# Performance work log

Measured on AMD Instinct MI355X. Metric: run time of the kernel, lower is better.

Reference implementation:

```python
import math
import jax
import jax.numpy as jnp
import numpy as np

B, S, S_IMG, D, H, MAX_SEQ = 8, 1024, 1, 1024, 16, 1024
HD = D // H


def setup_inputs() -> dict:
    key = jax.random.key(0)
    ks = jax.random.split(key, 8)
    w = 0.02  # GPT-2 init scale keeps softmax well-conditioned
    return {
        "hidden_states": jax.random.normal(ks[0], (B, S, D), jnp.float32),
        "attention_mask": jnp.ones((B, 1, 1, S + S_IMG), jnp.float32),
        "image_hidden_states": jax.random.normal(ks[1], (B, S_IMG, D), jnp.float32),
        "Wc_attn": jax.random.normal(ks[2], (D, 3 * D), jnp.float32) * w,  # Conv1D: x @ W + b
        "bc_attn": jnp.zeros((3 * D,), jnp.float32),
        "Wc_proj": jax.random.normal(ks[3], (D, D), jnp.float32) * w,
        "bc_proj": jnp.zeros((D,), jnp.float32),
        "Wuk": jax.random.normal(ks[4], (D, D), jnp.float32) * w,  # nn.Linear weight: x @ W.T
        "Wuv": jax.random.normal(ks[5], (D, D), jnp.float32) * w,
    }


def _split_heads(x):
    b, s, _ = x.shape
    return x.reshape(b, s, H, HD).transpose(0, 2, 1, 3)  # [B,H,S,hd]


def reference(hidden_states, attention_mask, image_hidden_states,
              Wc_attn, bc_attn, Wc_proj, bc_proj, Wuk, Wuv):
    # c_attn (Conv1D): x @ W + b, then split into q,k,v
    qkv = hidden_states @ Wc_attn + bc_attn
    q, k, v = jnp.split(qkv, 3, axis=-1)
    q, k, v = _split_heads(q), _split_heads(k), _split_heads(v)

    # image KV via bias-free Linear layers, appended to text KV (layer_past=None)
    k_img = _split_heads(image_hidden_states @ Wuk.T)
    v_img = _split_heads(image_hidden_states @ Wuv.T)
    k = jnp.concatenate([k, k_img], axis=2)
    v = jnp.concatenate([v, v_img], axis=2)

    Q, K = q.shape[2], k.shape[2]
    scores = jnp.einsum("bhqd,bhkd->bhqk", q, k) / math.sqrt(HD)

    # causal mask: tril(ones(max_seq_len, max_seq_len+1)) sliced to [Q,K]
    causal = jnp.tril(jnp.ones((MAX_SEQ, MAX_SEQ + 1), bool))[None, None, :Q, :K]
    scores = jnp.where(causal, scores, jnp.float32(-1e9))
    scores = jnp.where(attention_mask == 0, jnp.float32(-1e4), scores)

    p_attn = jax.nn.softmax(scores, axis=-1)  # dropout p=0 -> identity
    x = jnp.einsum("bhqk,bhkd->bhqd", p_attn, v)
    x = x.transpose(0, 2, 1, 3).reshape(hidden_states.shape[0], Q, D)
    return x @ Wc_proj + bc_proj
```

## Files before the change

### kernel.cpp

```cpp
#include <hip/hip_runtime.h>


#define DEVINL __device__ __forceinline__

typedef __attribute__((ext_vector_type(8))) short bf16x8;
typedef __attribute__((ext_vector_type(4))) float f32x4;
typedef __attribute__((ext_vector_type(16))) float f32x16;
typedef __attribute__((ext_vector_type(4))) unsigned int u32x4;

DEVINL unsigned short f2bf(float f) {
  unsigned u = __float_as_uint(f);
  u += 0x7fffu + ((u >> 16) & 1u);
  return (unsigned short)(u >> 16);
}

DEVINL void gload_lds16(const void* g, void* l) {
  __builtin_amdgcn_global_load_lds(
      (const __attribute__((address_space(1))) void*)g,
      (__attribute__((address_space(3))) void*)l, 16, 0, 0);
}

#define BARRIER() asm volatile("s_barrier" ::: "memory")

__global__ void cast_f32_bf16(const float* __restrict__ in,
                              unsigned short* __restrict__ out, int n4) {
  int i = blockIdx.x * blockDim.x + threadIdx.x;
  if (i >= n4) return;
  float4 f = ((const float4*)in)[i];
  uint2 o;
  o.x = (unsigned)f2bf(f.x) | ((unsigned)f2bf(f.y) << 16);
  o.y = (unsigned)f2bf(f.z) | ((unsigned)f2bf(f.w) << 16);
  ((uint2*)out)[i] = o;
}

__global__ void transpose_cast(const float* __restrict__ in,
                               unsigned short* __restrict__ out,
                               int rows, int cols) {
  __shared__ unsigned short tile[32][33];
  int bx = blockIdx.x * 32, by = blockIdx.y * 32;
  int tx = threadIdx.x, ty = threadIdx.y;
#pragma unroll
  for (int i = 0; i < 32; i += 8)
    tile[ty + i][tx] = f2bf(in[(size_t)(by + ty + i) * cols + bx + tx]);
  __syncthreads();
#pragma unroll
  for (int i = 0; i < 32; i += 8)
    out[(size_t)(bx + ty + i) * rows + by + tx] = tile[tx][ty + i];
}


DEVINL void stage_tile(const unsigned short* __restrict__ A,
                       const unsigned short* __restrict__ Bt, int m0, int n0,
                       int kt, int buf, int t, int w, unsigned char* lds) {
  const int base = buf * 16384;
#pragma unroll
  for (int i = 0; i < 2; i++) {
    const int idx = i * 256 + t;
    const int r = idx >> 2, p = idx & 3;
    const int c = p ^ ((r >> 1) & 3);
    gload_lds16(A + (size_t)(m0 + r) * 1024 + kt * 32 + c * 8,
                lds + base + (i * 256 + w * 64) * 16);
  }
#pragma unroll
  for (int i = 0; i < 2; i++) {
    const int idx = i * 256 + t;
    const int r = idx >> 2, p = idx & 3;
    const int c = p ^ ((r >> 1) & 3);
    gload_lds16(Bt + (size_t)(n0 + r) * 1024 + kt * 32 + c * 8,
                lds + base + 8192 + (i * 256 + w * 64) * 16);
  }
}

DEVINL bf16x8 readA2(const unsigned char* lds, int buf, int m, int wr, int lr,
                     int lg) {
  const int row = wr * 64 + m * 16 + lr;
  const int off = (lg ^ ((row >> 1) & 3)) << 4;
  return *(const bf16x8*)(lds + buf * 16384 + row * 64 + off);
}
DEVINL bf16x8 readB2(const unsigned char* lds, int buf, int n, int wc, int lr,
                     int lg) {
  const int row = wc * 64 + n * 16 + lr;
  const int off = (lg ^ ((row >> 1) & 3)) << 4;
  return *(const bf16x8*)(lds + buf * 16384 + 8192 + row * 64 + off);
}

DEVINL void gemm_core(const unsigned short* __restrict__ A,
                      const unsigned short* __restrict__ Bt, int m0, int n0,
                      unsigned char* lds, f32x4 (&acc)[4][4]) {
  const int t = threadIdx.x, w = t >> 6, l = t & 63, lr = l & 15, lg = l >> 4;
  const int wr = w >> 1, wc = w & 1;
  const int NT = 32;

  stage_tile(A, Bt, m0, n0, 0, 0, t, w, lds);
  stage_tile(A, Bt, m0, n0, 1, 1, t, w, lds);
  asm volatile("s_waitcnt vmcnt(4)" ::: "memory");
  __builtin_amdgcn_sched_barrier(0);
  BARRIER();

#pragma unroll 1
  for (int j = 0; j < NT; ++j) {
    const int buf = j % 3;
    if (j + 2 < NT) stage_tile(A, Bt, m0, n0, j + 2, (j + 2) % 3, t, w, lds);
    bf16x8 af[4], bf[4];
#pragma unroll
    for (int m = 0; m < 4; m++) af[m] = readA2(lds, buf, m, wr, lr, lg);
#pragma unroll
    for (int n = 0; n < 4; n++) bf[n] = readB2(lds, buf, n, wc, lr, lg);
    __builtin_amdgcn_s_setprio(1);
#pragma unroll
    for (int m = 0; m < 4; m++)
#pragma unroll
      for (int n = 0; n < 4; n++)
        acc[m][n] = __builtin_amdgcn_mfma_f32_16x16x32_bf16(af[m], bf[n],
                                                            acc[m][n], 0, 0, 0);
    __builtin_amdgcn_s_setprio(0);
    if (j + 1 < NT) {
      if (j + 2 < NT) {
        asm volatile("s_waitcnt vmcnt(4)" ::: "memory");
      } else {
        asm volatile("s_waitcnt vmcnt(0)" ::: "memory");
      }
      __builtin_amdgcn_sched_barrier(0);
      BARRIER();
    }
  }
}

DEVINL void tile_coords(int& m0, int& n0) {
  const int x = blockIdx.x & 7;
  const int local = blockIdx.x >> 3;
  const int mi = local & 7, ni = local >> 3;
  m0 = (x * 8 + mi) * 128;
  n0 = ni * 128;
}

__global__ __launch_bounds__(256, 3) void gemm_qkv(
    const unsigned short* __restrict__ A, const unsigned short* __restrict__ Bt,
    const float* __restrict__ bias, unsigned short* __restrict__ Qb,
    unsigned short* __restrict__ Kb, unsigned short* __restrict__ VTb) {
  __shared__ __align__(16) unsigned char lds[49152];
  f32x4 acc[4][4];
#pragma unroll
  for (int m = 0; m < 4; m++)
#pragma unroll
    for (int n = 0; n < 4; n++)
#pragma unroll
      for (int e = 0; e < 4; e++) acc[m][n][e] = 0.f;
  int m0, n0;
  tile_coords(m0, n0);
  gemm_core(A, Bt, m0, n0, lds, acc);

  const int t = threadIdx.x, w = t >> 6, l = t & 63, lr = l & 15, lg = l >> 4;
  const int wr = w >> 1, wc = w & 1;
  const int region = n0 >> 10;
  const int h0 = (n0 & 1023) >> 6;

  __syncthreads();
  unsigned short* epi = (unsigned short*)lds;
#pragma unroll
  for (int n = 0; n < 4; n++) {
    const int c = wc * 64 + n * 16 + lr;
    const float bv = bias[n0 + c];
#pragma unroll
    for (int m = 0; m < 4; m++)
#pragma unroll
      for (int e = 0; e < 4; e++) {
        const int r = wr * 64 + m * 16 + lg * 4 + e;
        const unsigned short val = f2bf(acc[m][n][e] + bv);
        if (region < 2) epi[r * 136 + c] = val;
        else            epi[c * 136 + r] = val;
      }
  }
  __syncthreads();

  const int row = t & 127, half = t >> 7;
  const unsigned short* src = epi + row * 136 + half * 64;
  if (region < 2) {
    unsigned short* dbuf = (region == 0) ? Qb : Kb;
    const int sg = m0 + row, b = sg >> 10, si = sg & 1023;
    unsigned short* dst =
        dbuf + (((size_t)b * 16 + h0 + half) * 1024 + si) * 64;
#pragma unroll
    for (int i = 0; i < 8; i++) ((u32x4*)dst)[i] = *(const u32x4*)(src + i * 8);
  } else {
    const int b = m0 >> 10;
    const int s0 = (m0 & 1023) + half * 64;
    const int head = h0 + (row >> 6), hdl = row & 63;
    unsigned short* dst =
        VTb + (((size_t)b * 16 + head) * 64 + hdl) * 1024 + s0;
#pragma unroll
    for (int i = 0; i < 8; i++) ((u32x4*)dst)[i] = *(const u32x4*)(src + i * 8);
  }
}

__global__ __launch_bounds__(256, 3) void gemm_proj(
    const unsigned short* __restrict__ A, const unsigned short* __restrict__ Bt,
    const float* __restrict__ bias, float* __restrict__ out) {
  __shared__ __align__(16) unsigned char lds[49152];
  f32x4 acc[4][4];
#pragma unroll
  for (int m = 0; m < 4; m++)
#pragma unroll
    for (int n = 0; n < 4; n++)
#pragma unroll
      for (int e = 0; e < 4; e++) acc[m][n][e] = 0.f;
  int m0, n0;
  tile_coords(m0, n0);
  gemm_core(A, Bt, m0, n0, lds, acc);
  const int t = threadIdx.x, w = t >> 6, l = t & 63, lr = l & 15, lg = l >> 4;
  const int wr = w >> 1, wc = w & 1;
#pragma unroll
  for (int n = 0; n < 4; n++) {
    const int col = n0 + wc * 64 + n * 16 + lr;
    const float bv = bias[col];
#pragma unroll
    for (int m = 0; m < 4; m++)
#pragma unroll
      for (int e = 0; e < 4; e++) {
        const int row = m0 + wr * 64 + m * 16 + lg * 4 + e;
        out[(size_t)row * 1024 + col] = acc[m][n][e] + bv;
      }
  }
}

__global__ __launch_bounds__(256) void attn_kernel(
    const unsigned short* __restrict__ Qb, const unsigned short* __restrict__ Kb,
    const unsigned short* __restrict__ VTb, unsigned short* __restrict__ Xb) {
  __shared__ float lsums[4][32];
  const int bh = blockIdx.x;
  const int t = threadIdx.x, w = t >> 6, l = t & 63;
  const int r = l & 31, hi = l >> 5;
  const int q0 = blockIdx.y * 128 + w * 32;

  bf16x8 qf[4];
  const unsigned short* qp = Qb + ((size_t)bh * 1024 + q0 + r) * 64 + hi * 8;
#pragma unroll
  for (int ks = 0; ks < 4; ks++) qf[ks] = *(const bf16x8*)(qp + ks * 16);

  f32x16 o0, o1;
#pragma unroll
  for (int e = 0; e < 16; e++) { o0[e] = 0.f; o1[e] = 0.f; }
  float lsum = 0.f;

  const unsigned short* kbase = Kb + ((size_t)bh * 1024 + r) * 64 + hi * 8;
  const unsigned short* vb0 = VTb + ((size_t)(bh * 64 + r)) * 1024 + hi * 8;
  const unsigned short* vb1 = vb0 + (size_t)32 * 1024;
  const int nt = (q0 >> 5) + 1;

  for (int tt = 0; tt < nt; ++tt) {
    const int j0 = tt * 32;
    f32x16 s;
#pragma unroll
    for (int e = 0; e < 16; e++) s[e] = 0.f;
    __builtin_amdgcn_s_setprio(1);
#pragma unroll
    for (int ks = 0; ks < 4; ks++) {
      bf16x8 kf = *(const bf16x8*)(kbase + (size_t)j0 * 64 + ks * 16);
      s = __builtin_amdgcn_mfma_f32_32x32x16_bf16(kf, qf[ks], s, 0, 0, 0);
    }
    __builtin_amdgcn_s_setprio(0);
    const bool diag = (tt == nt - 1);
    float p[16];
    float ls = 0.f;
#pragma unroll
    for (int e = 0; e < 16; e++) {
      const int jr = (e & 3) + 8 * (e >> 2) + 4 * hi;
      float pv = __expf(s[e] * 0.125f);
      if (diag && jr > r) pv = 0.f;
      p[e] = pv;
      ls += pv;
    }
    lsum += ls;
    unsigned wv[8];
#pragma unroll
    for (int g = 0; g < 4; g++) {
      wv[2 * g]     = (unsigned)f2bf(p[4 * g])     | ((unsigned)f2bf(p[4 * g + 1]) << 16);
      wv[2 * g + 1] = (unsigned)f2bf(p[4 * g + 2]) | ((unsigned)f2bf(p[4 * g + 3]) << 16);
    }
#pragma unroll
    for (int pr = 0; pr < 4; pr++) {
      const int ia = (pr & 1) + (pr >> 1) * 4;
      const int ib = ia + 2;
      unsigned a = wv[ia], b = wv[ib];
      unsigned ta = (unsigned)__shfl_xor((int)a, 32, 64);
      unsigned tb = (unsigned)__shfl_xor((int)b, 32, 64);
      wv[ia] = hi ? tb : a;
      wv[ib] = hi ? b : ta;
    }
    u32x4 w0, w1;
    w0[0] = wv[0]; w0[1] = wv[1]; w0[2] = wv[2]; w0[3] = wv[3];
    w1[0] = wv[4]; w1[1] = wv[5]; w1[2] = wv[6]; w1[3] = wv[7];
    bf16x8 pa0 = __builtin_bit_cast(bf16x8, w0);
    bf16x8 pa1 = __builtin_bit_cast(bf16x8, w1);

    bf16x8 v00 = *(const bf16x8*)(vb0 + j0);
    bf16x8 v01 = *(const bf16x8*)(vb0 + j0 + 16);
    bf16x8 v10 = *(const bf16x8*)(vb1 + j0);
    bf16x8 v11 = *(const bf16x8*)(vb1 + j0 + 16);
    __builtin_amdgcn_s_setprio(1);
    o0 = __builtin_amdgcn_mfma_f32_32x32x16_bf16(pa0, v00, o0, 0, 0, 0);
    o0 = __builtin_amdgcn_mfma_f32_32x32x16_bf16(pa1, v01, o0, 0, 0, 0);
    o1 = __builtin_amdgcn_mfma_f32_32x32x16_bf16(pa0, v10, o1, 0, 0, 0);
    o1 = __builtin_amdgcn_mfma_f32_32x32x16_bf16(pa1, v11, o1, 0, 0, 0);
    __builtin_amdgcn_s_setprio(0);
  }

  float ltot = lsum + __shfl_xor(lsum, 32, 64);
  if (l < 32) lsums[w][l] = ltot;
  __syncthreads();

  const int bb = bh >> 4, h = bh & 15;
#pragma unroll
  for (int e = 0; e < 16; e++) {
    const int rw = (e & 3) + 8 * (e >> 2) + 4 * hi;
    const float inv = 1.0f / lsums[w][rw];
    unsigned short* xp = Xb + ((size_t)bb * 1024 + q0 + rw) * 1024 + h * 64 + r;
    xp[0]  = f2bf(o0[e] * inv);
    xp[32] = f2bf(o1[e] * inv);
  }
}

extern "C" void kernel_launch(void* const* d_in, const int* in_sizes, int n_in,
                              void* d_out, int out_size, void* d_ws,
                              size_t ws_size, hipStream_t stream) {
  const float* hidden = (const float*)d_in[0];
  const float* Wattn = (const float*)d_in[3];
  const float* battn = (const float*)d_in[4];
  const float* Wproj = (const float*)d_in[5];
  const float* bproj = (const float*)d_in[6];

  unsigned short* hB  = (unsigned short*)d_ws;
  unsigned short* WaT = hB + (size_t)8192 * 1024;
  unsigned short* WpT = WaT + (size_t)3072 * 1024;
  unsigned short* Qb  = WpT + (size_t)1024 * 1024;
  unsigned short* Kb  = Qb + (size_t)8192 * 1024;
  unsigned short* VTb = Kb + (size_t)8192 * 1024;
  unsigned short* Xb  = hB;

  cast_f32_bf16<<<8192, 256, 0, stream>>>(hidden, hB, 2097152);
  transpose_cast<<<dim3(96, 32), dim3(32, 8), 0, stream>>>(Wattn, WaT, 1024, 3072);
  transpose_cast<<<dim3(32, 32), dim3(32, 8), 0, stream>>>(Wproj, WpT, 1024, 1024);
  gemm_qkv<<<1536, 256, 0, stream>>>(hB, WaT, battn, Qb, Kb, VTb);
  attn_kernel<<<dim3(128, 8), 256, 0, stream>>>(Qb, Kb, VTb, Xb);
  gemm_proj<<<512, 256, 0, stream>>>(Xb, WpT, bproj, (float*)d_out);
}
```

Measured before the change: 187.2 us.

## Widen GEMM tiles to 128x256 and reorder attention grid with diagonal specialization

Both GEMMs now use 128x256 output tiles: each wave computes 4x8 MFMA fragments and stages twice as much B data per k-step, with LDS buffers and occupancy bounds resized to match. The QKV epilogue is rewritten so each thread writes two heads, or a full 128-wide V^T row. This targets more operand reuse per LDS load and fewer blocks, in exchange for higher register and LDS pressure and lower occupancy. In attention, the grid axes are swapped so consecutive blocks share a batch-head, the causal-diagonal tile is split into a templated specialization, and a block barrier before the normalization reads is removed.

```diff
diff --git a/kernel.cpp b/kernel.cpp
--- a/kernel.cpp
+++ b/kernel.cpp
@@ -52,7 +52,7 @@
 DEVINL void stage_tile(const unsigned short* __restrict__ A,
                        const unsigned short* __restrict__ Bt, int m0, int n0,
                        int kt, int buf, int t, int w, unsigned char* lds) {
-  const int base = buf * 16384;
+  const int base = buf * 24576;
 #pragma unroll
   for (int i = 0; i < 2; i++) {
     const int idx = i * 256 + t;
@@ -62,7 +62,7 @@
                 lds + base + (i * 256 + w * 64) * 16);
   }
 #pragma unroll
-  for (int i = 0; i < 2; i++) {
+  for (int i = 0; i < 4; i++) {
     const int idx = i * 256 + t;
     const int r = idx >> 2, p = idx & 3;
     const int c = p ^ ((r >> 1) & 3);
@@ -75,25 +75,25 @@
                      int lg) {
   const int row = wr * 64 + m * 16 + lr;
   const int off = (lg ^ ((row >> 1) & 3)) << 4;
-  return *(const bf16x8*)(lds + buf * 16384 + row * 64 + off);
+  return *(const bf16x8*)(lds + buf * 24576 + row * 64 + off);
 }
 DEVINL bf16x8 readB2(const unsigned char* lds, int buf, int n, int wc, int lr,
                      int lg) {
-  const int row = wc * 64 + n * 16 + lr;
+  const int row = wc * 128 + n * 16 + lr;
   const int off = (lg ^ ((row >> 1) & 3)) << 4;
-  return *(const bf16x8*)(lds + buf * 16384 + 8192 + row * 64 + off);
+  return *(const bf16x8*)(lds + buf * 24576 + 8192 + row * 64 + off);
 }
 
 DEVINL void gemm_core(const unsigned short* __restrict__ A,
                       const unsigned short* __restrict__ Bt, int m0, int n0,
-                      unsigned char* lds, f32x4 (&acc)[4][4]) {
+                      unsigned char* lds, f32x4 (&acc)[4][8]) {
   const int t = threadIdx.x, w = t >> 6, l = t & 63, lr = l & 15, lg = l >> 4;
   const int wr = w >> 1, wc = w & 1;
   const int NT = 32;
 
   stage_tile(A, Bt, m0, n0, 0, 0, t, w, lds);
   stage_tile(A, Bt, m0, n0, 1, 1, t, w, lds);
-  asm volatile("s_waitcnt vmcnt(4)" ::: "memory");
+  asm volatile("s_waitcnt vmcnt(6)" ::: "memory");
   __builtin_amdgcn_sched_barrier(0);
   BARRIER();
 
@@ -101,22 +101,22 @@
   for (int j = 0; j < NT; ++j) {
     const int buf = j % 3;
     if (j + 2 < NT) stage_tile(A, Bt, m0, n0, j + 2, (j + 2) % 3, t, w, lds);
-    bf16x8 af[4], bf[4];
+    bf16x8 af[4], bf[8];
 #pragma unroll
     for (int m = 0; m < 4; m++) af[m] = readA2(lds, buf, m, wr, lr, lg);
 #pragma unroll
-    for (int n = 0; n < 4; n++) bf[n] = readB2(lds, buf, n, wc, lr, lg);
+    for (int n = 0; n < 8; n++) bf[n] = readB2(lds, buf, n, wc, lr, lg);
     __builtin_amdgcn_s_setprio(1);
 #pragma unroll
     for (int m = 0; m < 4; m++)
 #pragma unroll
-      for (int n = 0; n < 4; n++)
+      for (int n = 0; n < 8; n++)
         acc[m][n] = __builtin_amdgcn_mfma_f32_16x16x32_bf16(af[m], bf[n],
                                                             acc[m][n], 0, 0, 0);
     __builtin_amdgcn_s_setprio(0);
     if (j + 1 < NT) {
       if (j + 2 < NT) {
-        asm volatile("s_waitcnt vmcnt(4)" ::: "memory");
+        asm volatile("s_waitcnt vmcnt(6)" ::: "memory");
       } else {
         asm volatile("s_waitcnt vmcnt(0)" ::: "memory");
       }
@@ -131,19 +131,19 @@
   const int local = blockIdx.x >> 3;
   const int mi = local & 7, ni = local >> 3;
   m0 = (x * 8 + mi) * 128;
-  n0 = ni * 128;
-}
-
-__global__ __launch_bounds__(256, 3) void gemm_qkv(
+  n0 = ni * 256;
+}
+
+__global__ __launch_bounds__(256, 2) void gemm_qkv(
     const unsigned short* __restrict__ A, const unsigned short* __restrict__ Bt,
     const float* __restrict__ bias, unsigned short* __restrict__ Qb,
     unsigned short* __restrict__ Kb, unsigned short* __restrict__ VTb) {
-  __shared__ __align__(16) unsigned char lds[49152];
-  f32x4 acc[4][4];
+  __shared__ __align__(16) unsigned char lds[73728];
+  f32x4 acc[4][8];
 #pragma unroll
   for (int m = 0; m < 4; m++)
 #pragma unroll
-    for (int n = 0; n < 4; n++)
+    for (int n = 0; n < 8; n++)
 #pragma unroll
       for (int e = 0; e < 4; e++) acc[m][n][e] = 0.f;
   int m0, n0;
@@ -157,51 +157,69 @@
 
   __syncthreads();
   unsigned short* epi = (unsigned short*)lds;
-#pragma unroll
-  for (int n = 0; n < 4; n++) {
-    const int c = wc * 64 + n * 16 + lr;
-    const float bv = bias[n0 + c];
-#pragma unroll
-    for (int m = 0; m < 4; m++)
-#pragma unroll
-      for (int e = 0; e < 4; e++) {
-        const int r = wr * 64 + m * 16 + lg * 4 + e;
-        const unsigned short val = f2bf(acc[m][n][e] + bv);
-        if (region < 2) epi[r * 136 + c] = val;
-        else            epi[c * 136 + r] = val;
-      }
+  if (region < 2) {
+#pragma unroll
+    for (int n = 0; n < 8; n++) {
+      const int c = wc * 128 + n * 16 + lr;
+      const float bv = bias[n0 + c];
+#pragma unroll
+      for (int m = 0; m < 4; m++)
+#pragma unroll
+        for (int e = 0; e < 4; e++) {
+          const int r = wr * 64 + m * 16 + lg * 4 + e;
+          epi[r * 264 + c] = f2bf(acc[m][n][e] + bv);
+        }
+    }
+  } else {
+#pragma unroll
+    for (int n = 0; n < 8; n++) {
+      const int c = wc * 128 + n * 16 + lr;
+      const float bv = bias[n0 + c];
+#pragma unroll
+      for (int m = 0; m < 4; m++)
+#pragma unroll
+        for (int e = 0; e < 4; e++) {
+          const int r = wr * 64 + m * 16 + lg * 4 + e;
+          epi[c * 136 + r] = f2bf(acc[m][n][e] + bv);
+        }
+    }
   }
   __syncthreads();
 
-  const int row = t & 127, half = t >> 7;
-  const unsigned short* src = epi + row * 136 + half * 64;
   if (region < 2) {
+    const int row = t & 127, half = t >> 7;
     unsigned short* dbuf = (region == 0) ? Qb : Kb;
     const int sg = m0 + row, b = sg >> 10, si = sg & 1023;
-    unsigned short* dst =
-        dbuf + (((size_t)b * 16 + h0 + half) * 1024 + si) * 64;
-#pragma unroll
-    for (int i = 0; i < 8; i++) ((u32x4*)dst)[i] = *(const u32x4*)(src + i * 8);
+#pragma unroll
+    for (int hh = 0; hh < 2; hh++) {
+      const int head = h0 + half * 2 + hh;
+      const unsigned short* src = epi + row * 264 + half * 128 + hh * 64;
+      unsigned short* dst = dbuf + (((size_t)b * 16 + head) * 1024 + si) * 64;
+#pragma unroll
+      for (int i = 0; i < 8; i++)
+        ((u32x4*)dst)[i] = *(const u32x4*)(src + i * 8);
+    }
   } else {
-    const int b = m0 >> 10;
-    const int s0 = (m0 & 1023) + half * 64;
-    const int head = h0 + (row >> 6), hdl = row & 63;
-    unsigned short* dst =
-        VTb + (((size_t)b * 16 + head) * 64 + hdl) * 1024 + s0;
-#pragma unroll
-    for (int i = 0; i < 8; i++) ((u32x4*)dst)[i] = *(const u32x4*)(src + i * 8);
-  }
-}
-
-__global__ __launch_bounds__(256, 3) void gemm_proj(
+    const int c = t;
+    const int head = h0 + (c >> 6), hd = c & 63;
+    const int b = m0 >> 10, s0 = m0 & 1023;
+    const unsigned short* src = epi + c * 136;
+    unsigned short* dst = VTb + (((size_t)b * 16 + head) * 64 + hd) * 1024 + s0;
+#pragma unroll
+    for (int i = 0; i < 16; i++)
+      ((u32x4*)dst)[i] = *(const u32x4*)(src + i * 8);
+  }
+}
+
+__global__ __launch_bounds__(256, 2) void gemm_proj(
     const unsigned short* __restrict__ A, const unsigned short* __restrict__ Bt,
     const float* __restrict__ bias, float* __restrict__ out) {
-  __shared__ __align__(16) unsigned char lds[49152];
-  f32x4 acc[4][4];
+  __shared__ __align__(16) unsigned char lds[73728];
+  f32x4 acc[4][8];
 #pragma unroll
   for (int m = 0; m < 4; m++)
 #pragma unroll
-    for (int n = 0; n < 4; n++)
+    for (int n = 0; n < 8; n++)
 #pragma unroll
       for (int e = 0; e < 4; e++) acc[m][n][e] = 0.f;
   int m0, n0;
@@ -210,8 +228,8 @@
   const int t = threadIdx.x, w = t >> 6, l = t & 63, lr = l & 15, lg = l >> 4;
   const int wr = w >> 1, wc = w & 1;
 #pragma unroll
-  for (int n = 0; n < 4; n++) {
-    const int col = n0 + wc * 64 + n * 16 + lr;
+  for (int n = 0; n < 8; n++) {
+    const int col = n0 + wc * 128 + n * 16 + lr;
     const float bv = bias[col];
 #pragma unroll
     for (int m = 0; m < 4; m++)
@@ -223,14 +241,76 @@
   }
 }
 
+template <bool DIAG>
+DEVINL void attn_tile(int j0, int r, int hi, const unsigned short* kbase,
+                      const unsigned short* vb0, const unsigned short* vb1,
+                      const bf16x8 (&qf)[4], f32x16& o0, f32x16& o1,
+                      float& lsum) {
+  f32x16 s;
+#pragma unroll
+  for (int e = 0; e < 16; e++) s[e] = 0.f;
+  __builtin_amdgcn_s_setprio(1);
+#pragma unroll
+  for (int ks = 0; ks < 4; ks++) {
+    bf16x8 kf = *(const bf16x8*)(kbase + (size_t)j0 * 64 + ks * 16);
+    s = __builtin_amdgcn_mfma_f32_32x32x16_bf16(kf, qf[ks], s, 0, 0, 0);
+  }
+  __builtin_amdgcn_s_setprio(0);
+  float p[16];
+  float ls = 0.f;
+#pragma unroll
+  for (int e = 0; e < 16; e++) {
+    float pv = __expf(s[e] * 0.125f);
+    if (DIAG) {
+      const int jr = (e & 3) + 8 * (e >> 2) + 4 * hi;
+      if (jr > r) pv = 0.f;
+    }
+    p[e] = pv;
+    ls += pv;
+  }
+  lsum += ls;
+  unsigned wv[8];
+#pragma unroll
+  for (int g = 0; g < 4; g++) {
+    wv[2 * g]     = (unsigned)f2bf(p[4 * g])     | ((unsigned)f2bf(p[4 * g + 1]) << 16);
+    wv[2 * g + 1] = (unsigned)f2bf(p[4 * g + 2]) | ((unsigned)f2bf(p[4 * g + 3]) << 16);
+  }
+#pragma unroll
+  for (int pr = 0; pr < 4; pr++) {
+    const int ia = (pr & 1) + (pr >> 1) * 4;
+    const int ib = ia + 2;
+    unsigned a = wv[ia], b = wv[ib];
+    unsigned ta = (unsigned)__shfl_xor((int)a, 32, 64);
+    unsigned tb = (unsigned)__shfl_xor((int)b, 32, 64);
+    wv[ia] = hi ? tb : a;
+    wv[ib] = hi ? b : ta;
+  }
+  u32x4 w0, w1;
+  w0[0] = wv[0]; w0[1] = wv[1]; w0[2] = wv[2]; w0[3] = wv[3];
+  w1[0] = wv[4]; w1[1] = wv[5]; w1[2] = wv[6]; w1[3] = wv[7];
+  bf16x8 pa0 = __builtin_bit_cast(bf16x8, w0);
+  bf16x8 pa1 = __builtin_bit_cast(bf16x8, w1);
+
+  bf16x8 v00 = *(const bf16x8*)(vb0 + j0);
+  bf16x8 v01 = *(const bf16x8*)(vb0 + j0 + 16);
+  bf16x8 v10 = *(const bf16x8*)(vb1 + j0);
+  bf16x8 v11 = *(const bf16x8*)(vb1 + j0 + 16);
+  __builtin_amdgcn_s_setprio(1);
+  o0 = __builtin_amdgcn_mfma_f32_32x32x16_bf16(pa0, v00, o0, 0, 0, 0);
+  o0 = __builtin_amdgcn_mfma_f32_32x32x16_bf16(pa1, v01, o0, 0, 0, 0);
+  o1 = __builtin_amdgcn_mfma_f32_32x32x16_bf16(pa0, v10, o1, 0, 0, 0);
+  o1 = __builtin_amdgcn_mfma_f32_32x32x16_bf16(pa1, v11, o1, 0, 0, 0);
+  __builtin_amdgcn_s_setprio(0);
+}
+
 __global__ __launch_bounds__(256) void attn_kernel(
     const unsigned short* __restrict__ Qb, const unsigned short* __restrict__ Kb,
     const unsigned short* __restrict__ VTb, unsigned short* __restrict__ Xb) {
   __shared__ float lsums[4][32];
-  const int bh = blockIdx.x;
+  const int bh = blockIdx.y;
   const int t = threadIdx.x, w = t >> 6, l = t & 63;
   const int r = l & 31, hi = l >> 5;
-  const int q0 = blockIdx.y * 128 + w * 32;
+  const int q0 = blockIdx.x * 128 + w * 32;
 
   bf16x8 qf[4];
   const unsigned short* qp = Qb + ((size_t)bh * 1024 + q0 + r) * 64 + hi * 8;
@@ -247,67 +327,12 @@
   const unsigned short* vb1 = vb0 + (size_t)32 * 1024;
   const int nt = (q0 >> 5) + 1;
 
-  for (int tt = 0; tt < nt; ++tt) {
-    const int j0 = tt * 32;
-    f32x16 s;
-#pragma unroll
-    for (int e = 0; e < 16; e++) s[e] = 0.f;
-    __builtin_amdgcn_s_setprio(1);
-#pragma unroll
-    for (int ks = 0; ks < 4; ks++) {
-      bf16x8 kf = *(const bf16x8*)(kbase + (size_t)j0 * 64 + ks * 16);
-      s = __builtin_amdgcn_mfma_f32_32x32x16_bf16(kf, qf[ks], s, 0, 0, 0);
-    }
-    __builtin_amdgcn_s_setprio(0);
-    const bool diag = (tt == nt - 1);
-    float p[16];
-    float ls = 0.f;
-#pragma unroll
-    for (int e = 0; e < 16; e++) {
-      const int jr = (e & 3) + 8 * (e >> 2) + 4 * hi;
-      float pv = __expf(s[e] * 0.125f);
-      if (diag && jr > r) pv = 0.f;
-      p[e] = pv;
-      ls += pv;
-    }
-    lsum += ls;
-    unsigned wv[8];
-#pragma unroll
-    for (int g = 0; g < 4; g++) {
-      wv[2 * g]     = (unsigned)f2bf(p[4 * g])     | ((unsigned)f2bf(p[4 * g + 1]) << 16);
-      wv[2 * g + 1] = (unsigned)f2bf(p[4 * g + 2]) | ((unsigned)f2bf(p[4 * g + 3]) << 16);
-    }
-#pragma unroll
-    for (int pr = 0; pr < 4; pr++) {
-      const int ia = (pr & 1) + (pr >> 1) * 4;
-      const int ib = ia + 2;
-      unsigned a = wv[ia], b = wv[ib];
-      unsigned ta = (unsigned)__shfl_xor((int)a, 32, 64);
-      unsigned tb = (unsigned)__shfl_xor((int)b, 32, 64);
-      wv[ia] = hi ? tb : a;
-      wv[ib] = hi ? b : ta;
-    }
-    u32x4 w0, w1;
-    w0[0] = wv[0]; w0[1] = wv[1]; w0[2] = wv[2]; w0[3] = wv[3];
-    w1[0] = wv[4]; w1[1] = wv[5]; w1[2] = wv[6]; w1[3] = wv[7];
-    bf16x8 pa0 = __builtin_bit_cast(bf16x8, w0);
-    bf16x8 pa1 = __builtin_bit_cast(bf16x8, w1);
-
-    bf16x8 v00 = *(const bf16x8*)(vb0 + j0);
-    bf16x8 v01 = *(const bf16x8*)(vb0 + j0 + 16);
-    bf16x8 v10 = *(const bf16x8*)(vb1 + j0);
-    bf16x8 v11 = *(const bf16x8*)(vb1 + j0 + 16);
-    __builtin_amdgcn_s_setprio(1);
-    o0 = __builtin_amdgcn_mfma_f32_32x32x16_bf16(pa0, v00, o0, 0, 0, 0);
-    o0 = __builtin_amdgcn_mfma_f32_32x32x16_bf16(pa1, v01, o0, 0, 0, 0);
-    o1 = __builtin_amdgcn_mfma_f32_32x32x16_bf16(pa0, v10, o1, 0, 0, 0);
-    o1 = __builtin_amdgcn_mfma_f32_32x32x16_bf16(pa1, v11, o1, 0, 0, 0);
-    __builtin_amdgcn_s_setprio(0);
-  }
+  for (int tt = 0; tt < nt - 1; ++tt)
+    attn_tile<false>(tt * 32, r, hi, kbase, vb0, vb1, qf, o0, o1, lsum);
+  attn_tile<true>((nt - 1) * 32, r, hi, kbase, vb0, vb1, qf, o0, o1, lsum);
 
   float ltot = lsum + __shfl_xor(lsum, 32, 64);
   if (l < 32) lsums[w][l] = ltot;
-  __syncthreads();
 
   const int bb = bh >> 4, h = bh & 15;
 #pragma unroll
@@ -340,7 +365,7 @@
   cast_f32_bf16<<<8192, 256, 0, stream>>>(hidden, hB, 2097152);
   transpose_cast<<<dim3(96, 32), dim3(32, 8), 0, stream>>>(Wattn, WaT, 1024, 3072);
   transpose_cast<<<dim3(32, 32), dim3(32, 8), 0, stream>>>(Wproj, WpT, 1024, 1024);
-  gemm_qkv<<<1536, 256, 0, stream>>>(hB, WaT, battn, Qb, Kb, VTb);
-  attn_kernel<<<dim3(128, 8), 256, 0, stream>>>(Qb, Kb, VTb, Xb);
-  gemm_proj<<<512, 256, 0, stream>>>(Xb, WpT, bproj, (float*)d_out);
-}
+  gemm_qkv<<<768, 256, 0, stream>>>(hB, WaT, battn, Qb, Kb, VTb);
+  attn_kernel<<<dim3(8, 128), 256, 0, stream>>>(Qb, Kb, VTb, Xb);
+  gemm_proj<<<256, 256, 0, stream>>>(Xb, WpT, bproj, (float*)d_out);
+}
```

New measurement: 224.5 us. 20.0% more time.
